# Kernel optimization log

Measured on AMD Instinct MI355X. Metric: run time of the kernel, lower is better.

## Reference

```python
import jax, jax.numpy as jnp
import numpy as np

N, E, HID, HEADS, EDIM = 32768, 262144, 64, 4, 3
C = HID  # per-head out channels (concat=False -> mean over heads)


def setup_inputs() -> dict:
    key = jax.random.key(0)
    ks = jax.random.split(key, 24)
    g = lambda k, shape, s=1.0: jax.random.normal(k, shape, jnp.float32) * s
    s_lin = 1.0 / np.sqrt(HID)
    s_edge = 1.0 / np.sqrt(EDIM)
    s_att = 1.0 / np.sqrt(C)
    inp = {
        "t": jnp.zeros((1,), jnp.float32),
        "h": g(ks[0], (N, HID)),
        "edge_index": jax.random.randint(ks[1], (2, E), 0, N, jnp.int32),
        "edge_attr": g(ks[2], (E, EDIM)),
        "W1": g(ks[3], (HID, HEADS * C), s_lin),
        "We1": g(ks[4], (EDIM, HEADS * C), s_edge),
        "att_src1": g(ks[5], (HEADS, C), s_att),
        "att_dst1": g(ks[6], (HEADS, C), s_att),
        "att_edge1": g(ks[7], (HEADS, C), s_att),
        "b1": jnp.zeros((C,), jnp.float32),
        "ln_g1": jnp.ones((HID,), jnp.float32),
        "ln_b1": jnp.zeros((HID,), jnp.float32),
        # last GAT layer's lin weight is scaled by 0.1 in __init__
        "W2": g(ks[8], (HID, HEADS * C), s_lin) * 0.1,
        "We2": g(ks[9], (EDIM, HEADS * C), s_edge),
        "att_src2": g(ks[10], (HEADS, C), s_att),
        "att_dst2": g(ks[11], (HEADS, C), s_att),
        "att_edge2": g(ks[12], (HEADS, C), s_att),
        "b2": jnp.zeros((C,), jnp.float32),
        "ln_g2": jnp.ones((HID,), jnp.float32),
        "ln_b2": jnp.zeros((HID,), jnp.float32),
    }
    return inp


def _gat_layer(z, src, dst, edge_attr, W, We, a_src, a_dst, a_edge, b):
    # PyG GATConv(edge_dim>0, concat=False, add_self_loops=False), eval mode (no dropout)
    x = (z @ W).reshape(-1, HEADS, C)                      # [N,H,C]
    alpha_s = jnp.einsum("nhc,hc->nh", x, a_src)           # [N,H]
    alpha_d = jnp.einsum("nhc,hc->nh", x, a_dst)           # [N,H]
    e = (edge_attr @ We).reshape(-1, HEADS, C)             # [E,H,C]
    alpha_e = jnp.einsum("ehc,hc->eh", e, a_edge)          # [E,H]
    logit = jax.nn.leaky_relu(alpha_s[src] + alpha_d[dst] + alpha_e, 0.2)  # [E,H]
    # segment softmax over incoming edges of each destination node
    m = jax.lax.stop_gradient(jax.ops.segment_max(logit, dst, num_segments=N))
    ex = jnp.exp(logit - m[dst])
    denom = jax.ops.segment_sum(ex, dst, num_segments=N)
    alpha = ex / (denom[dst] + 1e-16)                      # [E,H]
    msg = x[src] * alpha[..., None]                        # [E,H,C] gather + weight
    out = jax.ops.segment_sum(msg, dst, num_segments=N)    # [N,H,C] scatter-add
    return out.mean(axis=1) + b                            # head mean + bias -> [N,C]


def _layernorm(x, g, b, eps=1e-5):
    mu = x.mean(-1, keepdims=True)
    var = ((x - mu) ** 2).mean(-1, keepdims=True)
    return (x - mu) * jax.lax.rsqrt(var + eps) * g + b


def reference(t, h, edge_index, edge_attr, W1, We1, att_src1, att_dst1, att_edge1, b1,
              ln_g1, ln_b1, W2, We2, att_src2, att_dst2, att_edge2, b2, ln_g2, ln_b2):
    del t  # autonomous ODE func: t unused
    src, dst = edge_index[0], edge_index[1]
    z = h
    z = jax.nn.silu(_layernorm(_gat_layer(z, src, dst, edge_attr, W1, We1, att_src1, att_dst1, att_edge1, b1), ln_g1, ln_b1))
    z = jax.nn.silu(_layernorm(_gat_layer(z, src, dst, edge_attr, W2, We2, att_src2, att_dst2, att_edge2, b2), ln_g2, ln_b2))
    return z
```

## Files before the change

kernel.cpp:

```cpp
#include <hip/hip_runtime.h>
#include <math.h>

#define HIDDEN 64
#define HEADS 4
#define HC 256
#define CAP 64

typedef __attribute__((ext_vector_type(8))) short short8;
typedef __attribute__((ext_vector_type(4))) float f32x4;

__device__ __forceinline__ unsigned short f2bf(float f) {
    unsigned int u = __float_as_uint(f);
    u += 0x7fffu + ((u >> 16) & 1u);
    return (unsigned short)(u >> 16);
}

__device__ __forceinline__ unsigned short f2h(float f) {
    _Float16 h = (_Float16)f;
    return *(unsigned short*)&h;
}

__device__ __forceinline__ float h2f(unsigned int u) {
    unsigned short s = (unsigned short)u;
    _Float16 h = *(_Float16*)&s;
    return (float)h;
}

__device__ __forceinline__ float bflo(unsigned int u) { return __uint_as_float(u << 16); }
__device__ __forceinline__ float bfhi(unsigned int u) { return __uint_as_float(u & 0xffff0000u); }

__global__ __launch_bounds__(256) void k_fused(const int* __restrict__ dst,
                                               const int* __restrict__ src,
                                               const float* __restrict__ ea,
                                               const float* __restrict__ h,
                                               const float* __restrict__ W1f,
                                               const float* __restrict__ W2f,
                                               const float* __restrict__ We1,
                                               const float* __restrict__ ae1,
                                               const float* __restrict__ We2,
                                               const float* __restrict__ ae2,
                                               const float* __restrict__ ats1,
                                               const float* __restrict__ atd1,
                                               const float* __restrict__ ats2,
                                               const float* __restrict__ atd2,
                                               int* __restrict__ counts,
                                               uint2* __restrict__ eb,
                                               ushort* __restrict__ zb,
                                               ushort* __restrict__ wst1,
                                               ushort* __restrict__ wst2,
                                               float* __restrict__ wsv,
                                               float* __restrict__ wr, int E) {
    int t = threadIdx.x, b = blockIdx.x;
    if (b < 1024) {
        int e = b * 256 + t;
        if (e < E) {
            int d = dst[e];
            int c = atomicAdd(&counts[d], 1);
            if (c < CAP) {
                size_t slot = (size_t)d * CAP + c;
                unsigned int lo = (unsigned int)(src[e] & 0xffff)
                                | ((unsigned int)f2h(ea[e * 3 + 0]) << 16);
                unsigned int hi = (unsigned int)f2h(ea[e * 3 + 1])
                                | ((unsigned int)f2h(ea[e * 3 + 2]) << 16);
                eb[slot] = make_uint2(lo, hi);
            }
        }
    } else if (b < 3072) {
        int i = (b - 1024) * 256 + t;
        float4 v = ((const float4*)h)[i];
        ushort4 o;
        o.x = f2bf(v.x); o.y = f2bf(v.y); o.z = f2bf(v.z); o.w = f2bf(v.w);
        ((ushort4*)zb)[i] = o;
    } else if (b < 3200) {
        int j = (b - 3072) * 256 + t;
        const float* W = (j < 16384) ? W1f : W2f;
        ushort* wst = (j < 16384) ? wst1 : wst2;
        int i = j & 16383;
        int c = i >> 8, k = i & 255;
        wst[i] = f2bf(0.25f * W[(k & 63) * HC + (k >> 6) * 64 + c]);
    } else if (b < 3204) {
        int r = b - 3200;
        const float* W = (r >> 1) ? W2f : W1f;
        const float* at;
        if (r == 0) at = ats1; else if (r == 1) at = atd1;
        else if (r == 2) at = ats2; else at = atd2;
        int hh = t >> 6, k = t & 63;
        const float4* wrow = (const float4*)&W[k * HC + hh * 64];
        const float4* arow = (const float4*)&at[hh * 64];
        float v = 0.f;
#pragma unroll
        for (int c4 = 0; c4 < 16; ++c4) {
            float4 wv = wrow[c4], av = arow[c4];
            v += wv.x * av.x + wv.y * av.y + wv.z * av.z + wv.w * av.w;
        }
        wsv[r * 256 + hh * 64 + k] = v;
    } else {
        int wv = t >> 6, lane = t & 63;
#pragma unroll
        for (int it = 0; it < 6; ++it) {
            int comb = wv + it * 4;
            int layer = comb / 12;
            int dh = comb % 12;
            int d = dh >> 2, hh = dh & 3;
            const float* We = layer ? We2 : We1;
            const float* at = layer ? ae2 : ae1;
            float v = We[d * HC + hh * HIDDEN + lane] * at[hh * HIDDEN + lane];
            for (int o = 32; o > 0; o >>= 1) v += __shfl_down(v, o);
            if (lane == 0) wr[layer * 16 + d * HEADS + hh] = v;
        }
    }
}

__global__ __launch_bounds__(256) void k_alpha(const ushort* __restrict__ zb,
                                               const float* __restrict__ wsv,
                                               float* __restrict__ as_,
                                               float* __restrict__ ad_) {
    __shared__ float ls[512];
    int t = threadIdx.x;
    ls[t] = wsv[t];
    ls[t + 256] = wsv[t + 256];
    __syncthreads();
    int n = blockIdx.x * 256 + t;
    const ushort* zr = zb + (size_t)n * HIDDEN;
    float as[4] = {0.f, 0.f, 0.f, 0.f};
    float ad[4] = {0.f, 0.f, 0.f, 0.f};
#pragma unroll
    for (int ks = 0; ks < 8; ++ks) {
        uint4 v = *(const uint4*)(zr + ks * 8);
        unsigned int uu[4] = {v.x, v.y, v.z, v.w};
#pragma unroll
        for (int p = 0; p < 4; ++p) {
            float f0 = bflo(uu[p]), f1 = bfhi(uu[p]);
            int k = ks * 8 + p * 2;
#pragma unroll
            for (int hh = 0; hh < 4; ++hh) {
                as[hh] += f0 * ls[hh * 64 + k] + f1 * ls[hh * 64 + k + 1];
                ad[hh] += f0 * ls[256 + hh * 64 + k] + f1 * ls[256 + hh * 64 + k + 1];
            }
        }
    }
    *(float4*)&as_[n * 4] = make_float4(as[0], as[1], as[2], as[3]);
    *(float4*)&ad_[n * 4] = make_float4(ad[0], ad[1], ad[2], ad[3]);
}

__global__ __launch_bounds__(256, 4) void k_aggout(
        const ushort* __restrict__ zb, const uint2* __restrict__ eb,
        const int* __restrict__ counts,
        const float* __restrict__ as_, const float* __restrict__ ad_,
        const float* __restrict__ wrl,
        const ushort* __restrict__ wst, const float* __restrict__ bias,
        const float* __restrict__ lng, const float* __restrict__ lnb,
        const float* __restrict__ wsv2,
        float* __restrict__ as2, float* __restrict__ ad2,
        float* __restrict__ outf, ushort* __restrict__ outb, int N) {
    __shared__ ushort sagg[16][264];
    int lane = threadIdx.x & 63;
    int wave = threadIdx.x >> 6;
    int h = lane >> 4, sub = lane & 15;
    int nbase = blockIdx.x * 16;

    float w0 = wrl[h], w1 = wrl[4 + h], w2 = wrl[8 + h];

    int degs[4]; float ad4s[4]; int bases[4];
#pragma unroll
    for (int i = 0; i < 4; ++i) {
        int n = nbase + wave * 4 + i;
        int d = counts[n];
        degs[i] = (d > CAP) ? CAP : d;
        ad4s[i] = ad_[(size_t)n * 4 + h];
        bases[i] = n * CAP;
    }

    uint2 rec[4];
#pragma unroll
    for (int i = 0; i < 4; ++i) rec[i] = eb[bases[i] + sub];

    int s_sub[4]; float aq[4];
#pragma unroll
    for (int i = 0; i < 4; ++i)
        s_sub[i] = (sub < degs[i]) ? (int)(rec[i].x & 0xffffu) : 0;
#pragma unroll
    for (int i = 0; i < 4; ++i) aq[i] = as_[(size_t)s_sub[i] * 4 + h];
    float wgt[4];
#pragma unroll
    for (int i = 0; i < 4; ++i) {
        float wv = 0.f;
        if (sub < degs[i]) {
            float lg = aq[i] + ad4s[i]
                     + h2f(rec[i].x >> 16) * w0
                     + h2f(rec[i].y) * w1
                     + h2f(rec[i].y >> 16) * w2;
            lg = (lg >= 0.f) ? lg : 0.2f * lg;
            wv = __expf(lg);
        }
        wgt[i] = wv;
    }

#pragma unroll 1
    for (int i = 0; i < 4; ++i) {
        int nl = wave * 4 + i;
        int deg = degs[i];
        float ssum = wgt[i];
        float acc[4][4];
#pragma unroll
        for (int a = 0; a < 4; ++a)
#pragma unroll
            for (int j = 0; j < 4; ++j) acc[a][j] = 0.f;

        int m0 = (deg > 16) ? 16 : deg;
        for (int j4 = 0; j4 < m0; j4 += 4) {
            int eidx = j4 + h;
            int s_g = __shfl(s_sub[i], eidx);
            uint2 zv = *(const uint2*)&zb[(size_t)s_g * HIDDEN + sub * 4];
            float z0 = bflo(zv.x), z1 = bfhi(zv.x);
            float z2v = bflo(zv.y), z3 = bfhi(zv.y);
#pragma unroll
            for (int hh = 0; hh < 4; ++hh) {
                float wh = __shfl(wgt[i], hh * 16 + eidx);
                acc[hh][0] += wh * z0;
                acc[hh][1] += wh * z1;
                acc[hh][2] += wh * z2v;
                acc[hh][3] += wh * z3;
            }
        }

        for (int cs = 16; cs < deg; cs += 16) {
            int idx = cs + sub;
            int st = 0; float wt = 0.f;
            if (idx < deg) {
                uint2 rt = eb[bases[i] + idx];
                st = (int)(rt.x & 0xffffu);
                float lg = as_[(size_t)st * 4 + h] + ad4s[i]
                         + h2f(rt.x >> 16) * w0 + h2f(rt.y) * w1
                         + h2f(rt.y >> 16) * w2;
                lg = (lg >= 0.f) ? lg : 0.2f * lg;
                wt = __expf(lg);
            }
            ssum += wt;
            int jb = deg - cs; if (jb > 16) jb = 16;
            for (int j4 = 0; j4 < jb; j4 += 4) {
                int eidx = j4 + h;
                int s_g = __shfl(st, eidx);
                uint2 zv = *(const uint2*)&zb[(size_t)s_g * HIDDEN + sub * 4];
                float z0 = bflo(zv.x), z1 = bfhi(zv.x);
                float z2v = bflo(zv.y), z3 = bfhi(zv.y);
#pragma unroll
                for (int hh = 0; hh < 4; ++hh) {
                    float wh = __shfl(wt, hh * 16 + eidx);
                    acc[hh][0] += wh * z0;
                    acc[hh][1] += wh * z1;
                    acc[hh][2] += wh * z2v;
                    acc[hh][3] += wh * z3;
                }
            }
        }

#pragma unroll
        for (int o = 1; o < 16; o <<= 1) ssum += __shfl_xor(ssum, o);
        float winv = 1.f / (ssum + 1e-16f);
#pragma unroll
        for (int a = 0; a < 4; ++a)
#pragma unroll
            for (int j = 0; j < 4; ++j) {
                acc[a][j] += __shfl_xor(acc[a][j], 16);
                acc[a][j] += __shfl_xor(acc[a][j], 32);
            }
        float sel[4];
#pragma unroll
        for (int j = 0; j < 4; ++j)
            sel[j] = (h == 0) ? acc[0][j] : (h == 1) ? acc[1][j]
                   : (h == 2) ? acc[2][j] : acc[3][j];
        uint2 pk;
        pk.x = (unsigned)f2bf(sel[0] * winv) | ((unsigned)f2bf(sel[1] * winv) << 16);
        pk.y = (unsigned)f2bf(sel[2] * winv) | ((unsigned)f2bf(sel[3] * winv) << 16);
        *(uint2*)&sagg[nl][h * 64 + sub * 4] = pk;
    }
    __syncthreads();

    if (wave == 0) {
        int q = lane & 15, quad = lane >> 4;
        short8 a[8];
#pragma unroll
        for (int ks = 0; ks < 8; ++ks)
            a[ks] = *(const short8*)&sagg[q][quad * 8 + ks * 32];

        f32x4 acc[4];
#pragma unroll
        for (int nt = 0; nt < 4; ++nt) {
            const ushort* brow = wst + (size_t)(nt * 16 + q) * HC + quad * 8;
            f32x4 c4 = {0.f, 0.f, 0.f, 0.f};
#pragma unroll
            for (int ks = 0; ks < 8; ++ks) {
                short8 bfr = *(const short8*)(brow + ks * 32);
                c4 = __builtin_amdgcn_mfma_f32_16x16x32_bf16(a[ks], bfr, c4, 0, 0, 0);
            }
            acc[nt] = c4;
        }

        float u[4][4], s1[4] = {0.f, 0.f, 0.f, 0.f};
#pragma unroll
        for (int nt = 0; nt < 4; ++nt) {
            float bv = bias[nt * 16 + q];
#pragma unroll
            for (int r = 0; r < 4; ++r) { u[nt][r] = acc[nt][r] + bv; s1[r] += u[nt][r]; }
        }
#pragma unroll
        for (int o = 1; o < 16; o <<= 1)
#pragma unroll
            for (int r = 0; r < 4; ++r) s1[r] += __shfl_xor(s1[r], o);
        float mu[4], s2[4] = {0.f, 0.f, 0.f, 0.f};
#pragma unroll
        for (int r = 0; r < 4; ++r) mu[r] = s1[r] * (1.f / 64.f);
#pragma unroll
        for (int nt = 0; nt < 4; ++nt)
#pragma unroll
            for (int r = 0; r < 4; ++r) { float d = u[nt][r] - mu[r]; s2[r] += d * d; }
#pragma unroll
        for (int o = 1; o < 16; o <<= 1)
#pragma unroll
            for (int r = 0; r < 4; ++r) s2[r] += __shfl_xor(s2[r], o);
        float rstd[4];
#pragma unroll
        for (int r = 0; r < 4; ++r) rstd[r] = rsqrtf(s2[r] * (1.f / 64.f) + 1e-5f);

        float rv[4][4];
#pragma unroll
        for (int nt = 0; nt < 4; ++nt) {
            float gv = lng[nt * 16 + q], bb = lnb[nt * 16 + q];
#pragma unroll
            for (int r = 0; r < 4; ++r) {
                float y = (u[nt][r] - mu[r]) * rstd[r] * gv + bb;
                rv[nt][r] = y / (1.f + __expf(-y));
            }
        }

        if (outb) {
#pragma unroll
            for (int nt = 0; nt < 4; ++nt)
#pragma unroll
                for (int r = 0; r < 4; ++r)
                    outb[(size_t)(nbase + quad * 4 + r) * HIDDEN + nt * 16 + q] = f2bf(rv[nt][r]);
            float vs[4][4] = {{0.f}}, vd[4][4] = {{0.f}};
#pragma unroll
            for (int hh = 0; hh < 4; ++hh)
#pragma unroll
                for (int nt = 0; nt < 4; ++nt) {
                    float wsc = wsv2[hh * 64 + nt * 16 + q];
                    float wdc = wsv2[256 + hh * 64 + nt * 16 + q];
#pragma unroll
                    for (int r = 0; r < 4; ++r) {
                        vs[r][hh] += rv[nt][r] * wsc;
                        vd[r][hh] += rv[nt][r] * wdc;
                    }
                }
#pragma unroll
            for (int o = 1; o < 16; o <<= 1)
#pragma unroll
                for (int r = 0; r < 4; ++r)
#pragma unroll
                    for (int hh = 0; hh < 4; ++hh) {
                        vs[r][hh] += __shfl_xor(vs[r][hh], o);
                        vd[r][hh] += __shfl_xor(vd[r][hh], o);
                    }
            if (q < 4) {
#pragma unroll
                for (int r = 0; r < 4; ++r) {
                    float sv = (q == 0) ? vs[r][0] : (q == 1) ? vs[r][1]
                             : (q == 2) ? vs[r][2] : vs[r][3];
                    float dv = (q == 0) ? vd[r][0] : (q == 1) ? vd[r][1]
                             : (q == 2) ? vd[r][2] : vd[r][3];
                    int n = nbase + quad * 4 + r;
                    as2[(size_t)n * 4 + q] = sv;
                    ad2[(size_t)n * 4 + q] = dv;
                }
            }
        } else {
#pragma unroll
            for (int nt = 0; nt < 4; ++nt)
#pragma unroll
                for (int r = 0; r < 4; ++r)
                    outf[(size_t)(nbase + quad * 4 + r) * HIDDEN + nt * 16 + q] = rv[nt][r];
        }
    }
}


extern "C" void kernel_launch(void* const* d_in, const int* in_sizes, int n_in,
                              void* d_out, int out_size, void* d_ws, size_t ws_size,
                              hipStream_t stream) {
    const float* h   = (const float*)d_in[1];
    const int*   ei  = (const int*)d_in[2];
    const float* ea  = (const float*)d_in[3];
    const float* W1  = (const float*)d_in[4];
    const float* We1 = (const float*)d_in[5];
    const float* as1 = (const float*)d_in[6];
    const float* ad1 = (const float*)d_in[7];
    const float* ae1 = (const float*)d_in[8];
    const float* b1  = (const float*)d_in[9];
    const float* lg1 = (const float*)d_in[10];
    const float* lb1 = (const float*)d_in[11];
    const float* W2  = (const float*)d_in[12];
    const float* We2 = (const float*)d_in[13];
    const float* as2 = (const float*)d_in[14];
    const float* ad2 = (const float*)d_in[15];
    const float* ae2 = (const float*)d_in[16];
    const float* b2  = (const float*)d_in[17];
    const float* lg2 = (const float*)d_in[18];
    const float* lb2 = (const float*)d_in[19];

    const int N = in_sizes[1] / HIDDEN;
    const int E = in_sizes[2] / 2;
    const int* srcp = ei;
    const int* dstp = ei + E;

    char* w = (char*)d_ws;
    ushort* zb    = (ushort*)w; w += (size_t)N * HIDDEN * 2;
    ushort* zb2   = (ushort*)w; w += (size_t)N * HIDDEN * 2;
    float* as_    = (float*)w;  w += (size_t)N * HEADS * 4;
    float* adv    = (float*)w;  w += (size_t)N * HEADS * 4;
    float* as2_   = (float*)w;  w += (size_t)N * HEADS * 4;
    float* ad2_   = (float*)w;  w += (size_t)N * HEADS * 4;
    ushort* wst1  = (ushort*)w; w += 16384 * 2;
    ushort* wst2  = (ushort*)w; w += 16384 * 2;
    float* wsv    = (float*)w;  w += 1024 * 4;
    float* wr     = (float*)w;  w += 128;
    int* counts   = (int*)w;    w += (size_t)N * 4;
    uint2* eb     = (uint2*)w;  w += (size_t)N * CAP * 8;

    hipMemsetAsync(counts, 0, (size_t)N * 4, stream);
    k_fused<<<3205, 256, 0, stream>>>(dstp, srcp, ea, h, W1, W2,
                                      We1, ae1, We2, ae2,
                                      as1, ad1, as2, ad2,
                                      counts, eb, zb, wst1, wst2, wsv, wr, E);

    k_alpha<<<N / 256, 256, 0, stream>>>(zb, wsv, as_, adv);

    k_aggout<<<N / 16, 256, 0, stream>>>(zb, eb, counts, as_, adv, wr,
                                         wst1, b1, lg1, lb1, wsv + 512,
                                         as2_, ad2_, nullptr, zb2, N);
    k_aggout<<<N / 16, 256, 0, stream>>>(zb2, eb, counts, as2_, ad2_, wr + 16,
                                         wst2, b2, lg2, lb2, nullptr,
                                         nullptr, nullptr, (float*)d_out, nullptr, N);
}
```

Baseline: 188.4 us.

## Fold alpha projection into prep and fuse both GAT layers via cooperative grid sync

Computes the layer-1 source/destination attention logits directly from fp32 h inside the prep kernel's conversion blocks, which removes the separate alpha kernel. Both aggregation layers now run in a single cooperative kernel of 1024 blocks, each handling two 16-node tiles per layer with a grid.sync between layers, cutting launches. If the cooperative launch fails, it falls back to two ordinary launches. The risks are reduced parallelism from 1024 persistent blocks and grid-sync overhead, and every conversion block redundantly recomputes the W·att projections.

```diff
diff --git a/kernel.cpp b/kernel.cpp
--- a/kernel.cpp
+++ b/kernel.cpp
@@ -1,5 +1,8 @@
 #include <hip/hip_runtime.h>
+#include <hip/hip_cooperative_groups.h>
 #include <math.h>
+
+namespace cg = cooperative_groups;
 
 #define HIDDEN 64
 #define HEADS 4
@@ -29,27 +32,29 @@
 __device__ __forceinline__ float bflo(unsigned int u) { return __uint_as_float(u << 16); }
 __device__ __forceinline__ float bfhi(unsigned int u) { return __uint_as_float(u & 0xffff0000u); }
 
-__global__ __launch_bounds__(256) void k_fused(const int* __restrict__ dst,
-                                               const int* __restrict__ src,
-                                               const float* __restrict__ ea,
-                                               const float* __restrict__ h,
-                                               const float* __restrict__ W1f,
-                                               const float* __restrict__ W2f,
-                                               const float* __restrict__ We1,
-                                               const float* __restrict__ ae1,
-                                               const float* __restrict__ We2,
-                                               const float* __restrict__ ae2,
-                                               const float* __restrict__ ats1,
-                                               const float* __restrict__ atd1,
-                                               const float* __restrict__ ats2,
-                                               const float* __restrict__ atd2,
-                                               int* __restrict__ counts,
-                                               uint2* __restrict__ eb,
-                                               ushort* __restrict__ zb,
-                                               ushort* __restrict__ wst1,
-                                               ushort* __restrict__ wst2,
-                                               float* __restrict__ wsv,
-                                               float* __restrict__ wr, int E) {
+__global__ __launch_bounds__(256) void k_prep(const int* __restrict__ dst,
+                                              const int* __restrict__ src,
+                                              const float* __restrict__ ea,
+                                              const float* __restrict__ h,
+                                              const float* __restrict__ W1f,
+                                              const float* __restrict__ W2f,
+                                              const float* __restrict__ We1,
+                                              const float* __restrict__ ae1,
+                                              const float* __restrict__ We2,
+                                              const float* __restrict__ ae2,
+                                              const float* __restrict__ ats1,
+                                              const float* __restrict__ atd1,
+                                              const float* __restrict__ ats2,
+                                              const float* __restrict__ atd2,
+                                              int* __restrict__ counts,
+                                              uint2* __restrict__ eb,
+                                              ushort* __restrict__ zb,
+                                              ushort* __restrict__ wst1,
+                                              ushort* __restrict__ wst2,
+                                              float* __restrict__ wsv,
+                                              float* __restrict__ wr,
+                                              float* __restrict__ as_,
+                                              float* __restrict__ ad_, int E) {
     int t = threadIdx.x, b = blockIdx.x;
     if (b < 1024) {
         int e = b * 256 + t;
@@ -66,11 +71,55 @@
             }
         }
     } else if (b < 3072) {
-        int i = (b - 1024) * 256 + t;
-        float4 v = ((const float4*)h)[i];
+        __shared__ float lws[512];
+        {
+            int hh = t >> 6, k = t & 63;
+            const float4* wrow = (const float4*)&W1f[k * HC + hh * 64];
+            const float4* srow = (const float4*)&ats1[hh * 64];
+            const float4* drow = (const float4*)&atd1[hh * 64];
+            float vs = 0.f, vd = 0.f;
+#pragma unroll
+            for (int c4 = 0; c4 < 16; ++c4) {
+                float4 wv = wrow[c4], sv = srow[c4], dv = drow[c4];
+                vs += wv.x * sv.x + wv.y * sv.y + wv.z * sv.z + wv.w * sv.w;
+                vd += wv.x * dv.x + wv.y * dv.y + wv.z * dv.z + wv.w * dv.w;
+            }
+            lws[t] = vs;
+            lws[256 + t] = vd;
+        }
+        __syncthreads();
+        int nl = t >> 4, cl = t & 15;
+        int n = (b - 1024) * 16 + nl;
+        float4 hv = *(const float4*)&h[(size_t)n * HIDDEN + cl * 4];
         ushort4 o;
-        o.x = f2bf(v.x); o.y = f2bf(v.y); o.z = f2bf(v.z); o.w = f2bf(v.w);
-        ((ushort4*)zb)[i] = o;
+        o.x = f2bf(hv.x); o.y = f2bf(hv.y); o.z = f2bf(hv.z); o.w = f2bf(hv.w);
+        ((ushort4*)zb)[n * 16 + cl] = o;
+        float pas[4], pad[4];
+#pragma unroll
+        for (int hh = 0; hh < 4; ++hh) {
+            int k0 = hh * 64 + cl * 4;
+            pas[hh] = hv.x * lws[k0] + hv.y * lws[k0 + 1]
+                    + hv.z * lws[k0 + 2] + hv.w * lws[k0 + 3];
+            pad[hh] = hv.x * lws[256 + k0] + hv.y * lws[256 + k0 + 1]
+                    + hv.z * lws[256 + k0 + 2] + hv.w * lws[256 + k0 + 3];
+        }
+#pragma unroll
+        for (int o2 = 1; o2 < 16; o2 <<= 1)
+#pragma unroll
+            for (int hh = 0; hh < 4; ++hh) {
+                pas[hh] += __shfl_xor(pas[hh], o2);
+                pad[hh] += __shfl_xor(pad[hh], o2);
+            }
+        if (cl < 4) {
+            float v = (cl == 0) ? pas[0] : (cl == 1) ? pas[1]
+                    : (cl == 2) ? pas[2] : pas[3];
+            as_[(size_t)n * 4 + cl] = v;
+        } else if (cl < 8) {
+            int c = cl - 4;
+            float v = (c == 0) ? pad[0] : (c == 1) ? pad[1]
+                    : (c == 2) ? pad[2] : pad[3];
+            ad_[(size_t)n * 4 + c] = v;
+        }
     } else if (b < 3200) {
         int j = (b - 3072) * 256 + t;
         const float* W = (j < 16384) ? W1f : W2f;
@@ -78,14 +127,11 @@
         int i = j & 16383;
         int c = i >> 8, k = i & 255;
         wst[i] = f2bf(0.25f * W[(k & 63) * HC + (k >> 6) * 64 + c]);
-    } else if (b < 3204) {
-        int r = b - 3200;
-        const float* W = (r >> 1) ? W2f : W1f;
-        const float* at;
-        if (r == 0) at = ats1; else if (r == 1) at = atd1;
-        else if (r == 2) at = ats2; else at = atd2;
+    } else if (b < 3202) {
+        int r = b - 3200 + 2;
+        const float* at = (r == 2) ? ats2 : atd2;
         int hh = t >> 6, k = t & 63;
-        const float4* wrow = (const float4*)&W[k * HC + hh * 64];
+        const float4* wrow = (const float4*)&W2f[k * HC + hh * 64];
         const float4* arow = (const float4*)&at[hh * 64];
         float v = 0.f;
 #pragma unroll
@@ -111,76 +157,42 @@
     }
 }
 
-__global__ __launch_bounds__(256) void k_alpha(const ushort* __restrict__ zb,
-                                               const float* __restrict__ wsv,
-                                               float* __restrict__ as_,
-                                               float* __restrict__ ad_) {
-    __shared__ float ls[512];
-    int t = threadIdx.x;
-    ls[t] = wsv[t];
-    ls[t + 256] = wsv[t + 256];
-    __syncthreads();
-    int n = blockIdx.x * 256 + t;
-    const ushort* zr = zb + (size_t)n * HIDDEN;
-    float as[4] = {0.f, 0.f, 0.f, 0.f};
-    float ad[4] = {0.f, 0.f, 0.f, 0.f};
-#pragma unroll
-    for (int ks = 0; ks < 8; ++ks) {
-        uint4 v = *(const uint4*)(zr + ks * 8);
-        unsigned int uu[4] = {v.x, v.y, v.z, v.w};
-#pragma unroll
-        for (int p = 0; p < 4; ++p) {
-            float f0 = bflo(uu[p]), f1 = bfhi(uu[p]);
-            int k = ks * 8 + p * 2;
-#pragma unroll
-            for (int hh = 0; hh < 4; ++hh) {
-                as[hh] += f0 * ls[hh * 64 + k] + f1 * ls[hh * 64 + k + 1];
-                ad[hh] += f0 * ls[256 + hh * 64 + k] + f1 * ls[256 + hh * 64 + k + 1];
-            }
-        }
-    }
-    *(float4*)&as_[n * 4] = make_float4(as[0], as[1], as[2], as[3]);
-    *(float4*)&ad_[n * 4] = make_float4(ad[0], ad[1], ad[2], ad[3]);
-}
-
-__global__ __launch_bounds__(256, 4) void k_aggout(
-        const ushort* __restrict__ zb, const uint2* __restrict__ eb,
-        const int* __restrict__ counts,
-        const float* __restrict__ as_, const float* __restrict__ ad_,
-        const float* __restrict__ wrl,
-        const ushort* __restrict__ wst, const float* __restrict__ bias,
-        const float* __restrict__ lng, const float* __restrict__ lnb,
-        const float* __restrict__ wsv2,
-        float* __restrict__ as2, float* __restrict__ ad2,
-        float* __restrict__ outf, ushort* __restrict__ outb, int N) {
-    __shared__ ushort sagg[16][264];
+struct LayerArgs {
+    const ushort* zsrc; const uint2* eb; const int* counts;
+    const float* asv; const float* adv; const float* wrl;
+    const ushort* wst; const float* bias; const float* lng; const float* lnb;
+    const float* wsv2; float* as2; float* ad2;
+    float* outf; ushort* outb;
+};
+
+__device__ __forceinline__ void aggout_tile(const LayerArgs& a, int nbase,
+                                            ushort (*sagg)[264]) {
     int lane = threadIdx.x & 63;
     int wave = threadIdx.x >> 6;
     int h = lane >> 4, sub = lane & 15;
-    int nbase = blockIdx.x * 16;
-
-    float w0 = wrl[h], w1 = wrl[4 + h], w2 = wrl[8 + h];
+
+    float w0 = a.wrl[h], w1 = a.wrl[4 + h], w2 = a.wrl[8 + h];
 
     int degs[4]; float ad4s[4]; int bases[4];
 #pragma unroll
     for (int i = 0; i < 4; ++i) {
         int n = nbase + wave * 4 + i;
-        int d = counts[n];
+        int d = a.counts[n];
         degs[i] = (d > CAP) ? CAP : d;
-        ad4s[i] = ad_[(size_t)n * 4 + h];
+        ad4s[i] = a.adv[(size_t)n * 4 + h];
         bases[i] = n * CAP;
     }
 
     uint2 rec[4];
 #pragma unroll
-    for (int i = 0; i < 4; ++i) rec[i] = eb[bases[i] + sub];
+    for (int i = 0; i < 4; ++i) rec[i] = a.eb[bases[i] + sub];
 
     int s_sub[4]; float aq[4];
 #pragma unroll
     for (int i = 0; i < 4; ++i)
         s_sub[i] = (sub < degs[i]) ? (int)(rec[i].x & 0xffffu) : 0;
 #pragma unroll
-    for (int i = 0; i < 4; ++i) aq[i] = as_[(size_t)s_sub[i] * 4 + h];
+    for (int i = 0; i < 4; ++i) aq[i] = a.asv[(size_t)s_sub[i] * 4 + h];
     float wgt[4];
 #pragma unroll
     for (int i = 0; i < 4; ++i) {
@@ -203,15 +215,15 @@
         float ssum = wgt[i];
         float acc[4][4];
 #pragma unroll
-        for (int a = 0; a < 4; ++a)
-#pragma unroll
-            for (int j = 0; j < 4; ++j) acc[a][j] = 0.f;
+        for (int aa = 0; aa < 4; ++aa)
+#pragma unroll
+            for (int j = 0; j < 4; ++j) acc[aa][j] = 0.f;
 
         int m0 = (deg > 16) ? 16 : deg;
         for (int j4 = 0; j4 < m0; j4 += 4) {
             int eidx = j4 + h;
             int s_g = __shfl(s_sub[i], eidx);
-            uint2 zv = *(const uint2*)&zb[(size_t)s_g * HIDDEN + sub * 4];
+            uint2 zv = *(const uint2*)&a.zsrc[(size_t)s_g * HIDDEN + sub * 4];
             float z0 = bflo(zv.x), z1 = bfhi(zv.x);
             float z2v = bflo(zv.y), z3 = bfhi(zv.y);
 #pragma unroll
@@ -228,9 +240,9 @@
             int idx = cs + sub;
             int st = 0; float wt = 0.f;
             if (idx < deg) {
-                uint2 rt = eb[bases[i] + idx];
+                uint2 rt = a.eb[bases[i] + idx];
                 st = (int)(rt.x & 0xffffu);
-                float lg = as_[(size_t)st * 4 + h] + ad4s[i]
+                float lg = a.asv[(size_t)st * 4 + h] + ad4s[i]
                          + h2f(rt.x >> 16) * w0 + h2f(rt.y) * w1
                          + h2f(rt.y >> 16) * w2;
                 lg = (lg >= 0.f) ? lg : 0.2f * lg;
@@ -241,7 +253,7 @@
             for (int j4 = 0; j4 < jb; j4 += 4) {
                 int eidx = j4 + h;
                 int s_g = __shfl(st, eidx);
-                uint2 zv = *(const uint2*)&zb[(size_t)s_g * HIDDEN + sub * 4];
+                uint2 zv = *(const uint2*)&a.zsrc[(size_t)s_g * HIDDEN + sub * 4];
                 float z0 = bflo(zv.x), z1 = bfhi(zv.x);
                 float z2v = bflo(zv.y), z3 = bfhi(zv.y);
 #pragma unroll
@@ -259,11 +271,11 @@
         for (int o = 1; o < 16; o <<= 1) ssum += __shfl_xor(ssum, o);
         float winv = 1.f / (ssum + 1e-16f);
 #pragma unroll
-        for (int a = 0; a < 4; ++a)
+        for (int aa = 0; aa < 4; ++aa)
 #pragma unroll
             for (int j = 0; j < 4; ++j) {
-                acc[a][j] += __shfl_xor(acc[a][j], 16);
-                acc[a][j] += __shfl_xor(acc[a][j], 32);
+                acc[aa][j] += __shfl_xor(acc[aa][j], 16);
+                acc[aa][j] += __shfl_xor(acc[aa][j], 32);
             }
         float sel[4];
 #pragma unroll
@@ -279,20 +291,20 @@
 
     if (wave == 0) {
         int q = lane & 15, quad = lane >> 4;
-        short8 a[8];
+        short8 av[8];
 #pragma unroll
         for (int ks = 0; ks < 8; ++ks)
-            a[ks] = *(const short8*)&sagg[q][quad * 8 + ks * 32];
+            av[ks] = *(const short8*)&sagg[q][quad * 8 + ks * 32];
 
         f32x4 acc[4];
 #pragma unroll
         for (int nt = 0; nt < 4; ++nt) {
-            const ushort* brow = wst + (size_t)(nt * 16 + q) * HC + quad * 8;
+            const ushort* brow = a.wst + (size_t)(nt * 16 + q) * HC + quad * 8;
             f32x4 c4 = {0.f, 0.f, 0.f, 0.f};
 #pragma unroll
             for (int ks = 0; ks < 8; ++ks) {
                 short8 bfr = *(const short8*)(brow + ks * 32);
-                c4 = __builtin_amdgcn_mfma_f32_16x16x32_bf16(a[ks], bfr, c4, 0, 0, 0);
+                c4 = __builtin_amdgcn_mfma_f32_16x16x32_bf16(av[ks], bfr, c4, 0, 0, 0);
             }
             acc[nt] = c4;
         }
@@ -300,7 +312,7 @@
         float u[4][4], s1[4] = {0.f, 0.f, 0.f, 0.f};
 #pragma unroll
         for (int nt = 0; nt < 4; ++nt) {
-            float bv = bias[nt * 16 + q];
+            float bv = a.bias[nt * 16 + q];
 #pragma unroll
             for (int r = 0; r < 4; ++r) { u[nt][r] = acc[nt][r] + bv; s1[r] += u[nt][r]; }
         }
@@ -326,7 +338,7 @@
         float rv[4][4];
 #pragma unroll
         for (int nt = 0; nt < 4; ++nt) {
-            float gv = lng[nt * 16 + q], bb = lnb[nt * 16 + q];
+            float gv = a.lng[nt * 16 + q], bb = a.lnb[nt * 16 + q];
 #pragma unroll
             for (int r = 0; r < 4; ++r) {
                 float y = (u[nt][r] - mu[r]) * rstd[r] * gv + bb;
@@ -334,19 +346,19 @@
             }
         }
 
-        if (outb) {
+        if (a.outb) {
 #pragma unroll
             for (int nt = 0; nt < 4; ++nt)
 #pragma unroll
                 for (int r = 0; r < 4; ++r)
-                    outb[(size_t)(nbase + quad * 4 + r) * HIDDEN + nt * 16 + q] = f2bf(rv[nt][r]);
+                    a.outb[(size_t)(nbase + quad * 4 + r) * HIDDEN + nt * 16 + q] = f2bf(rv[nt][r]);
             float vs[4][4] = {{0.f}}, vd[4][4] = {{0.f}};
 #pragma unroll
             for (int hh = 0; hh < 4; ++hh)
 #pragma unroll
                 for (int nt = 0; nt < 4; ++nt) {
-                    float wsc = wsv2[hh * 64 + nt * 16 + q];
-                    float wdc = wsv2[256 + hh * 64 + nt * 16 + q];
+                    float wsc = a.wsv2[hh * 64 + nt * 16 + q];
+                    float wdc = a.wsv2[256 + hh * 64 + nt * 16 + q];
 #pragma unroll
                     for (int r = 0; r < 4; ++r) {
                         vs[r][hh] += rv[nt][r] * wsc;
@@ -370,8 +382,8 @@
                     float dv = (q == 0) ? vd[r][0] : (q == 1) ? vd[r][1]
                              : (q == 2) ? vd[r][2] : vd[r][3];
                     int n = nbase + quad * 4 + r;
-                    as2[(size_t)n * 4 + q] = sv;
-                    ad2[(size_t)n * 4 + q] = dv;
+                    a.as2[(size_t)n * 4 + q] = sv;
+                    a.ad2[(size_t)n * 4 + q] = dv;
                 }
             }
         } else {
@@ -379,9 +391,25 @@
             for (int nt = 0; nt < 4; ++nt)
 #pragma unroll
                 for (int r = 0; r < 4; ++r)
-                    outf[(size_t)(nbase + quad * 4 + r) * HIDDEN + nt * 16 + q] = rv[nt][r];
-        }
-    }
+                    a.outf[(size_t)(nbase + quad * 4 + r) * HIDDEN + nt * 16 + q] = rv[nt][r];
+        }
+    }
+    __syncthreads();
+}
+
+__global__ __launch_bounds__(256, 4) void k_layers(LayerArgs L1, LayerArgs L2) {
+    __shared__ ushort sagg[16][264];
+    cg::grid_group grid = cg::this_grid();
+    aggout_tile(L1, (blockIdx.x * 2 + 0) * 16, sagg);
+    aggout_tile(L1, (blockIdx.x * 2 + 1) * 16, sagg);
+    grid.sync();
+    aggout_tile(L2, (blockIdx.x * 2 + 0) * 16, sagg);
+    aggout_tile(L2, (blockIdx.x * 2 + 1) * 16, sagg);
+}
+
+__global__ __launch_bounds__(256, 4) void k_layer_fb(LayerArgs a) {
+    __shared__ ushort sagg[16][264];
+    aggout_tile(a, blockIdx.x * 16, sagg);
 }
 
 
@@ -428,17 +456,22 @@
     uint2* eb     = (uint2*)w;  w += (size_t)N * CAP * 8;
 
     hipMemsetAsync(counts, 0, (size_t)N * 4, stream);
-    k_fused<<<3205, 256, 0, stream>>>(dstp, srcp, ea, h, W1, W2,
-                                      We1, ae1, We2, ae2,
-                                      as1, ad1, as2, ad2,
-                                      counts, eb, zb, wst1, wst2, wsv, wr, E);
-
-    k_alpha<<<N / 256, 256, 0, stream>>>(zb, wsv, as_, adv);
-
-    k_aggout<<<N / 16, 256, 0, stream>>>(zb, eb, counts, as_, adv, wr,
-                                         wst1, b1, lg1, lb1, wsv + 512,
-                                         as2_, ad2_, nullptr, zb2, N);
-    k_aggout<<<N / 16, 256, 0, stream>>>(zb2, eb, counts, as2_, ad2_, wr + 16,
-                                         wst2, b2, lg2, lb2, nullptr,
-                                         nullptr, nullptr, (float*)d_out, nullptr, N);
-}
+    k_prep<<<3203, 256, 0, stream>>>(dstp, srcp, ea, h, W1, W2,
+                                     We1, ae1, We2, ae2,
+                                     as1, ad1, as2, ad2,
+                                     counts, eb, zb, wst1, wst2, wsv, wr,
+                                     as_, adv, E);
+
+    LayerArgs L1 = { zb,  eb, counts, as_,  adv,  wr,      wst1, b1, lg1, lb1,
+                     wsv + 512, as2_, ad2_, nullptr, zb2 };
+    LayerArgs L2 = { zb2, eb, counts, as2_, ad2_, wr + 16, wst2, b2, lg2, lb2,
+                     nullptr, nullptr, nullptr, (float*)d_out, nullptr };
+
+    void* kargs[] = { (void*)&L1, (void*)&L2 };
+    hipError_t err = hipLaunchCooperativeKernel((const void*)k_layers, dim3(1024),
+                                                dim3(256), kargs, 0, stream);
+    if (err != hipSuccess) {
+        k_layer_fb<<<2048, 256, 0, stream>>>(L1);
+        k_layer_fb<<<2048, 256, 0, stream>>>(L2);
+    }
+}
```

New measurement: 382.3 us. +102.9%, slower.
